# Performance work log

Hardware: AMD Instinct MI355X
Metric: run time of the kernel (lower is better)

Reference implementation:

```python
import jax, jax.numpy as jnp
import numpy as np

BN_EPS = 1e-5

def _conv1x1(x, w, b=None):
    # x: [B,C,H,W], w: [O,C] -> [B,O,H,W]
    y = jnp.einsum('bchw,oc->bohw', x, w)
    if b is not None:
        y = y + b[None, :, None, None]
    return y

def _bn_silu(y, gamma, beta):
    # BN inference with running_mean=0, running_var=1, then SiLU
    scale = gamma / jnp.sqrt(1.0 + BN_EPS)
    y = y * scale[None, :, None, None] + beta[None, :, None, None]
    return jax.nn.silu(y)

def setup_inputs() -> dict:
    key = jax.random.key(0)
    ks = jax.random.split(key, 20)
    B, D, S = 32, 512, 32
    C = D // 2
    d = {}
    d['x'] = jax.random.normal(ks[0], (B, D, S, S), jnp.float32)
    d['cv1_w'] = jax.random.normal(ks[1], (C, D), jnp.float32) * (1.0 / np.sqrt(D))
    d['cv1_gamma'] = jax.random.uniform(ks[2], (C,), jnp.float32, 0.5, 1.5)
    d['cv1_beta'] = jax.random.normal(ks[3], (C,), jnp.float32) * 0.1
    d['q_w'] = jax.random.normal(ks[4], (C, C), jnp.float32) * (1.0 / np.sqrt(C))
    d['q_b'] = jax.random.normal(ks[5], (C,), jnp.float32) * 0.02
    d['k_w'] = jax.random.normal(ks[6], (C, C), jnp.float32) * (1.0 / np.sqrt(C))
    d['k_b'] = jax.random.normal(ks[7], (C,), jnp.float32) * 0.02
    d['v_w'] = jax.random.normal(ks[8], (C, C), jnp.float32) * (1.0 / np.sqrt(C))
    d['v_b'] = jax.random.normal(ks[9], (C,), jnp.float32) * 0.02
    d['e_w'] = jax.random.normal(ks[10], (C, C), jnp.float32) * (1.0 / np.sqrt(C))
    d['e_b'] = jax.random.normal(ks[11], (C,), jnp.float32) * 0.02
    d['rel_h'] = jax.random.normal(ks[12], (1, C, S, 1), jnp.float32)
    d['rel_w'] = jax.random.normal(ks[13], (1, C, 1, S), jnp.float32)
    d['cv2_w'] = jax.random.normal(ks[14], (D, C), jnp.float32) * (1.0 / np.sqrt(C))
    d['cv2_gamma'] = jax.random.uniform(ks[15], (D,), jnp.float32, 0.5, 1.5)
    d['cv2_beta'] = jax.random.normal(ks[16], (D,), jnp.float32) * 0.1
    return d

def reference(x, cv1_w, cv1_gamma, cv1_beta, q_w, q_b, k_w, k_b, v_w, v_b,
              e_w, e_b, rel_h, rel_w, cv2_w, cv2_gamma, cv2_beta):
    # cv1: 1x1 conv (no bias) + BN + SiLU
    x1 = _bn_silu(_conv1x1(x, cv1_w), cv1_gamma, cv1_beta)  # [B,C,H,W]
    B, C, H, W = x1.shape
    N = H * W
    q = _conv1x1(x1, q_w, q_b).reshape(B, C, N)
    k = _conv1x1(x1, k_w, k_b).reshape(B, C, N)
    v = _conv1x1(x1, v_w, v_b).reshape(B, C, N)
    e = _conv1x1(x1, e_w, e_b).reshape(B, C, N)
    # content-content: q^T k -> [B,N,N]
    cc = jnp.einsum('bci,bcj->bij', q, k)
    # content-position: (rel_h + rel_w) flattened to [C,N], times extra proj
    pos = (rel_h + rel_w).reshape(C, N)  # broadcast add -> [1,C,H,W] -> [C,N]
    cp = jnp.einsum('ci,bcj->bij', pos, e)  # [B,N,N]
    attn = jax.nn.softmax(cc + cp, axis=-1)
    # out[b,c,i] = sum_j v[b,c,j] * attn[b,i,j]
    out = jnp.einsum('bcj,bij->bci', v, attn).reshape(B, C, H, W)
    y = _bn_silu(_conv1x1(out, cv2_w), cv2_gamma, cv2_beta)
    return x + y
```

## Files before the change

kernel.cpp:

```cpp
#include <hip/hip_runtime.h>
#include <hip/hip_bf16.h>

typedef unsigned short u16;
typedef __attribute__((ext_vector_type(8))) _Float16 half8;
typedef __attribute__((ext_vector_type(4))) float f32x4;

__device__ __forceinline__ u16 f2h(float f) {
  _Float16 h = (_Float16)f;
  union { _Float16 h; u16 u; } a; a.h = h;
  return a.u;
}

__device__ __forceinline__ float h2f(u16 u) {
  union { _Float16 h; u16 u; } a; a.u = u;
  return (float)a.h;
}

__device__ __forceinline__ float silu_f(float y) {
  return y / (1.0f + __expf(-y));
}

__device__ __forceinline__ void glds16(const u16* g, u16* l) {
  __builtin_amdgcn_global_load_lds(
      (__attribute__((address_space(1))) unsigned*)(g),
      (__attribute__((address_space(3))) unsigned*)(l), 16, 0, 0);
}

enum { EPI_BNSILU_N = 0, EPI_QKEV, EPI_RAW_F16, EPI_BNSILU_RES_M };

template<int EPI, bool DUAL, int TILES, int GX>
__global__ __launch_bounds__(256, 3)
void gemm_nt(const u16* __restrict__ A, long long a_bs, int lda,
             const u16* __restrict__ A2,
             const u16* __restrict__ B, long long b_bs, int ldb,
             void* __restrict__ C0, long long c_bs, int ldc,
             void* __restrict__ C1, void* __restrict__ C2,
             int K,
             const float* __restrict__ p0, const float* __restrict__ p1,
             const float* __restrict__ res, long long res_bs)
{
  __shared__ u16 smem[16384];

  const int id = blockIdx.x;
  const int bz = (id & 7) + 8 * (id / (8 * TILES));
  const int tt = (id >> 3) % TILES;
  const int bm = tt % GX;
  const int bn = tt / GX;
  const u16* Ab = A + (long long)bz * a_bs;
  const u16* Bb = B + (long long)bz * b_bs;
  const int m0 = bm * 128;
  const int n0 = bn * 128;
  const int t = threadIdx.x;
  const int lane = t & 63;
  const int w = t >> 6;
  const int wm = (w & 1) * 64;
  const int wn = (w >> 1) * 64;
  const int q = lane >> 4;
  const int lr = lane & 15;

  f32x4 acc[4][4];
#pragma unroll
  for (int i = 0; i < 4; ++i)
#pragma unroll
    for (int j = 0; j < 4; ++j)
      acc[i][j] = (f32x4){0.f, 0.f, 0.f, 0.f};

  const int lrow = lane >> 2;
  const int kch = (lane & 3) ^ ((lane >> 2) & 3) ^ ((lane >> 4) & 3);
  const int lk = kch * 8;
  const u16* aR0 = Ab + (long long)(m0 + 32 * w + lrow) * lda + lk;
  const u16* aR1 = aR0 + 16LL * lda;
  const u16* bR0 = Bb + (long long)(n0 + 32 * w + lrow) * ldb + lk;
  const u16* bR1 = bR0 + 16LL * ldb;
  const u16* a2R0 = nullptr; const u16* a2R1 = nullptr;
  if constexpr (DUAL) {
    a2R0 = A2 + (long long)(m0 + 32 * w + lrow) * 256 + lk;
    a2R1 = a2R0 + 16LL * 256;
  }
  u16* la0 = smem + w * 1024;        u16* la1 = la0 + 512;
  u16* lb0 = smem + 8192 + w * 1024; u16* lb1 = lb0 + 512;
  const int fpos = (q ^ (lr & 3) ^ ((lr >> 2) & 3)) * 8;

  for (int k0 = 0; k0 < K; k0 += 64) {
    __syncthreads();
    if (!DUAL || k0 < 256) {
      glds16(aR0 + k0, la0);        glds16(aR1 + k0, la1);
      glds16(aR0 + k0 + 32, la0 + 4096); glds16(aR1 + k0 + 32, la1 + 4096);
    } else {
      glds16(a2R0 + (k0 - 256), la0);        glds16(a2R1 + (k0 - 256), la1);
      glds16(a2R0 + (k0 - 224), la0 + 4096); glds16(a2R1 + (k0 - 224), la1 + 4096);
    }
    glds16(bR0 + k0, lb0);        glds16(bR1 + k0, lb1);
    glds16(bR0 + k0 + 32, lb0 + 4096); glds16(bR1 + k0 + 32, lb1 + 4096);
    __syncthreads();
#pragma unroll
    for (int h = 0; h < 2; ++h) {
      half8 af[4], bfr[4];
#pragma unroll
      for (int i = 0; i < 4; ++i)
        af[i] = *(const half8*)&smem[h * 4096 + (wm + i * 16 + lr) * 32 + fpos];
#pragma unroll
      for (int j = 0; j < 4; ++j)
        bfr[j] = *(const half8*)&smem[8192 + h * 4096 + (wn + j * 16 + lr) * 32 + fpos];
#pragma unroll
      for (int i = 0; i < 4; ++i)
#pragma unroll
        for (int j = 0; j < 4; ++j)
          acc[i][j] = __builtin_amdgcn_mfma_f32_16x16x32_f16(af[i], bfr[j], acc[i][j], 0, 0, 0);
    }
  }

  if constexpr (EPI == EPI_BNSILU_N) {
    u16* Cg = (u16*)C0 + (long long)bz * c_bs;
#pragma unroll
    for (int i = 0; i < 4; ++i)
#pragma unroll
      for (int j = 0; j < 4; ++j)
#pragma unroll
        for (int r = 0; r < 4; ++r) {
          const int m = m0 + wm + i * 16 + q * 4 + r;
          const int n = n0 + wn + j * 16 + lr;
          float v = acc[i][j][r];
          v = silu_f(v * (p0[n] * 0.99999500003749969f) + p1[n]);
          Cg[(long long)m * ldc + n] = f2h(v);
        }
  } else if constexpr (EPI == EPI_RAW_F16) {
    u16* Cg = (u16*)C0 + (long long)bz * c_bs;
#pragma unroll
    for (int i = 0; i < 4; ++i)
#pragma unroll
      for (int j = 0; j < 4; ++j)
#pragma unroll
        for (int r = 0; r < 4; ++r) {
          const int m = m0 + wm + i * 16 + q * 4 + r;
          const int n = n0 + wn + j * 16 + lr;
          Cg[(long long)m * ldc + n] = f2h(acc[i][j][r]);
        }
  } else if constexpr (EPI == EPI_BNSILU_RES_M) {
    float* Cg = (float*)C0 + (long long)bz * c_bs;
    const float* rg = res + (long long)bz * res_bs;
#pragma unroll
    for (int i = 0; i < 4; ++i)
#pragma unroll
      for (int j = 0; j < 4; ++j)
#pragma unroll
        for (int r = 0; r < 4; ++r) {
          const int m = m0 + wm + i * 16 + q * 4 + r;
          const int n = n0 + wn + j * 16 + lr;
          float v = acc[i][j][r];
          v = silu_f(v * (p0[m] * 0.99999500003749969f) + p1[m]);
          const long long idx = (long long)m * ldc + n;
          Cg[idx] = v + rg[idx];
        }
  } else {
    const int seg = n0 >> 8;
    const int nb = n0 & 255;
    if (seg < 3) {
      u16* dst; long long bs; int ld2;
      if (seg == 0) { dst = (u16*)C0; bs = 262144; ld2 = 256; }
      else { dst = (u16*)C1 + (seg == 2 ? 256 : 0); bs = 524288; ld2 = 512; }
      dst += (long long)bz * bs;
#pragma unroll
      for (int i = 0; i < 4; ++i)
#pragma unroll
        for (int j = 0; j < 4; ++j)
#pragma unroll
          for (int r = 0; r < 4; ++r) {
            const int m = m0 + wm + i * 16 + q * 4 + r;
            const int col = wn + j * 16 + lr;
            float v = acc[i][j][r] + p0[n0 + col];
            dst[(long long)m * ld2 + nb + col] = f2h(v);
          }
    } else {
      u16* dst = (u16*)C2 + (long long)bz * 262144;
#pragma unroll
      for (int s = 0; s < 4; ++s) {
        const int rbase = s * 32;
        __syncthreads();
        if (wm == (rbase & 64)) {
          const int ibase = (rbase & 32) >> 4;
#pragma unroll
          for (int ii = 0; ii < 2; ++ii) {
            const int i = ibase + ii;
#pragma unroll
            for (int j = 0; j < 4; ++j)
#pragma unroll
              for (int r = 0; r < 4; ++r) {
                const int row32 = i * 16 + q * 4 + r - (rbase & 32);
                const int col = wn + j * 16 + lr;
                float v = acc[i][j][r] + p0[768 + nb + col];
                smem[row32 * 132 + col] = f2h(v);
              }
          }
        }
        __syncthreads();
#pragma unroll
        for (int p = 0; p < 2; ++p) {
          const int lin = p * 256 + t;
          const int c = lin >> 2;
          const int mc = lin & 3;
          u16 tmp[8];
#pragma unroll
          for (int r8 = 0; r8 < 8; ++r8)
            tmp[r8] = smem[(mc * 8 + r8) * 132 + c];
          *(half8*)&dst[(long long)(nb + c) * 1024 + m0 + rbase + mc * 8] =
              *(const half8*)tmp;
        }
      }
    }
  }
}

__global__ __launch_bounds__(256)
void transpose_x(const float* __restrict__ x, u16* __restrict__ xT) {
  __shared__ float tile[64][33];
  const int b = blockIdx.z;
  const int n0 = blockIdx.x * 32;
  const int d0 = blockIdx.y * 64;
  const int tx = threadIdx.x;
  const int ty = threadIdx.y;
  const float* src = x + (long long)b * 524288;
#pragma unroll
  for (int i = 0; i < 8; ++i)
    tile[ty + 8 * i][tx] = src[(long long)(d0 + ty + 8 * i) * 1024 + n0 + tx];
  __syncthreads();
  u16* dst = xT + (long long)b * 524288;
#pragma unroll
  for (int i = 0; i < 4; ++i) {
    const int n = ty + 8 * i;
    unsigned lo = (unsigned)f2h(tile[2 * tx][n]);
    unsigned hi = (unsigned)f2h(tile[2 * tx + 1][n]);
    *(unsigned*)&dst[(long long)(n0 + n) * 512 + d0 + 2 * tx] = lo | (hi << 16);
  }
}

__global__ __launch_bounds__(256)
void convert_w(const float* __restrict__ w1, const float* __restrict__ wq,
               const float* __restrict__ wk, const float* __restrict__ wv,
               const float* __restrict__ we, const float* __restrict__ w2,
               const float* __restrict__ bq, const float* __restrict__ bk,
               const float* __restrict__ be, const float* __restrict__ bv,
               u16* __restrict__ dstw, float* __restrict__ bbuf) {
  int id = blockIdx.x * 256 + threadIdx.x;
  if (id < 524288) {
    float v;
    if (id < 131072) v = w1[id];
    else if (id < 393216) {
      int s = id - 131072, o = s >> 8, c = s & 255;
      if (o < 256) v = wq[o * 256 + c];
      else if (o < 512) v = wk[(o - 256) * 256 + c];
      else if (o < 768) v = we[(o - 512) * 256 + c];
      else v = wv[(o - 768) * 256 + c];
    } else v = w2[id - 393216];
    dstw[id] = f2h(v);
  } else {
    int i = id - 524288;
    float v;
    if (i < 256) v = bq[i];
    else if (i < 512) v = bk[i - 256];
    else if (i < 768) v = be[i - 512];
    else v = bv[i - 768];
    bbuf[i] = v;
  }
}

__global__ __launch_bounds__(256)
void pos_compute(const float* __restrict__ rh, const float* __restrict__ rw,
                 u16* __restrict__ posT) {
  const int n = blockIdx.x;
  const int c = threadIdx.x;
  posT[n * 256 + c] = f2h(rh[c * 32 + (n >> 5)] + rw[c * 32 + (n & 31)]);
}

__global__ __launch_bounds__(256)
void softmax_rows(u16* __restrict__ logits) {
  __shared__ float red[8];
  u16* p = logits + (long long)blockIdx.x * 1024;
  const int t = threadIdx.x;
  ushort4 raw = ((const ushort4*)p)[t];
  float v0 = h2f(raw.x), v1 = h2f(raw.y), v2 = h2f(raw.z), v3 = h2f(raw.w);
  float mx = fmaxf(fmaxf(v0, v1), fmaxf(v2, v3));
#pragma unroll
  for (int off = 32; off > 0; off >>= 1) mx = fmaxf(mx, __shfl_down(mx, off));
  const int lane = t & 63, w = t >> 6;
  if (lane == 0) red[w] = mx;
  __syncthreads();
  mx = fmaxf(fmaxf(red[0], red[1]), fmaxf(red[2], red[3]));
  float e0 = __expf(v0 - mx), e1 = __expf(v1 - mx),
        e2 = __expf(v2 - mx), e3 = __expf(v3 - mx);
  float s = e0 + e1 + e2 + e3;
#pragma unroll
  for (int off = 32; off > 0; off >>= 1) s += __shfl_down(s, off);
  if (lane == 0) red[4 + w] = s;
  __syncthreads();
  const float inv = 1.0f / (red[4] + red[5] + red[6] + red[7]);
  ushort4 o;
  o.x = f2h(e0 * inv); o.y = f2h(e1 * inv); o.z = f2h(e2 * inv); o.w = f2h(e3 * inv);
  ((ushort4*)p)[t] = o;
}

extern "C" void kernel_launch(void* const* d_in, const int* in_sizes, int n_in,
                              void* d_out, int out_size, void* d_ws, size_t ws_size,
                              hipStream_t stream) {
  const float* x  = (const float*)d_in[0];
  const float* w1 = (const float*)d_in[1];
  const float* g1 = (const float*)d_in[2];
  const float* b1 = (const float*)d_in[3];
  const float* wq = (const float*)d_in[4];
  const float* bq = (const float*)d_in[5];
  const float* wk = (const float*)d_in[6];
  const float* bk = (const float*)d_in[7];
  const float* wv = (const float*)d_in[8];
  const float* bv = (const float*)d_in[9];
  const float* we = (const float*)d_in[10];
  const float* be = (const float*)d_in[11];
  const float* rh = (const float*)d_in[12];
  const float* rw = (const float*)d_in[13];
  const float* w2 = (const float*)d_in[14];
  const float* g2 = (const float*)d_in[15];
  const float* b2 = (const float*)d_in[16];
  float* out = (float*)d_out;
  char* ws = (char*)d_ws;

  u16* xT     = (u16*)(ws + 0);
  u16* x1t    = (u16*)(ws + 33554432);
  u16* qbuf   = (u16*)(ws + 50331648);
  u16* kcat   = (u16*)(ws + 67108864);
  u16* vbuf   = (u16*)(ws + 100663296);
  u16* outt   = (u16*)(ws + 117440512);
  u16* posT   = (u16*)(ws + 134217728);
  u16* wbuf   = (u16*)(ws + 134742016);
  float* bbuf = (float*)(ws + 135790592);
  u16* logits = (u16*)(ws + 142606336);

  u16* w1b    = wbuf;
  u16* wqkve  = wbuf + 131072;
  u16* w2b    = wbuf + 393216;

  transpose_x<<<dim3(32, 8, 32), dim3(32, 8), 0, stream>>>(x, xT);
  convert_w<<<dim3(2052), 256, 0, stream>>>(w1, wq, wk, wv, we, w2,
                                            bq, bk, be, bv, wbuf, bbuf);
  pos_compute<<<dim3(1024), 256, 0, stream>>>(rh, rw, posT);

  gemm_nt<EPI_BNSILU_N, false, 16, 8><<<dim3(512), 256, 0, stream>>>(
      xT, 524288LL, 512, nullptr, w1b, 0LL, 512,
      x1t, 262144LL, 256, nullptr, nullptr, 512, g1, b1, nullptr, 0LL);

  gemm_nt<EPI_QKEV, false, 64, 8><<<dim3(2048), 256, 0, stream>>>(
      x1t, 262144LL, 256, nullptr, wqkve, 0LL, 256,
      qbuf, 262144LL, 256, kcat, vbuf, 256, bbuf, nullptr, nullptr, 0LL);

  gemm_nt<EPI_RAW_F16, true, 64, 8><<<dim3(2048), 256, 0, stream>>>(
      qbuf, 262144LL, 256, posT, kcat, 524288LL, 512,
      logits, 1048576LL, 1024, nullptr, nullptr, 512, nullptr, nullptr, nullptr, 0LL);

  softmax_rows<<<dim3(32768), 256, 0, stream>>>(logits);

  gemm_nt<EPI_RAW_F16, false, 16, 8><<<dim3(512), 256, 0, stream>>>(
      logits, 1048576LL, 1024, nullptr, vbuf, 262144LL, 1024,
      outt, 262144LL, 256, nullptr, nullptr, 1024, nullptr, nullptr, nullptr, 0LL);

  gemm_nt<EPI_BNSILU_RES_M, false, 32, 4><<<dim3(1024), 256, 0, stream>>>(
      w2b, 0LL, 256, nullptr, outt, 262144LL, 256,
      out, 524288LL, 1024, nullptr, nullptr, 256, g2, b2, x, 524288LL);
}
```

Baseline: 330.7 us.

## Fuse softmax exponentiation and normalization into the attention-times-V GEMM

The softmax pass no longer rewrites the logits. It now only computes a per-row max and sum and stores them as a float2 stats buffer. The attn·V GEMM exponentiates the A fragments on the fly using the row max and scales the output by the inverse row sum in its epilogue. This removes a full read-modify-write of the fp16 logits tensor, at the cost of extra exp work inside the GEMM's inner loop. Each logits element is exponentiated once per N-tile, so this is repeated across tiles.

Result: slower. 352.2 us (+6.5%).

```diff
diff --git a/kernel.cpp b/kernel.cpp
--- a/kernel.cpp
+++ b/kernel.cpp
@@ -26,7 +26,7 @@
       (__attribute__((address_space(3))) unsigned*)(l), 16, 0, 0);
 }
 
-enum { EPI_BNSILU_N = 0, EPI_QKEV, EPI_RAW_F16, EPI_BNSILU_RES_M };
+enum { EPI_BNSILU_N = 0, EPI_QKEV, EPI_RAW_F16, EPI_BNSILU_RES_M, EPI_ATTNV };
 
 template<int EPI, bool DUAL, int TILES, int GX>
 __global__ __launch_bounds__(256, 3)
@@ -81,6 +81,13 @@
   u16* lb0 = smem + 8192 + w * 1024; u16* lb1 = lb0 + 512;
   const int fpos = (q ^ (lr & 3) ^ ((lr >> 2) & 3)) * 8;
 
+  float mrow[4] = {0.f, 0.f, 0.f, 0.f};
+  if constexpr (EPI == EPI_ATTNV) {
+    const float2* st = (const float2*)p0 + (long long)bz * 1024;
+#pragma unroll
+    for (int i = 0; i < 4; ++i) mrow[i] = st[m0 + wm + i * 16 + lr].x;
+  }
+
   for (int k0 = 0; k0 < K; k0 += 64) {
     __syncthreads();
     if (!DUAL || k0 < 256) {
@@ -102,6 +109,15 @@
 #pragma unroll
       for (int j = 0; j < 4; ++j)
         bfr[j] = *(const half8*)&smem[8192 + h * 4096 + (wn + j * 16 + lr) * 32 + fpos];
+      if constexpr (EPI == EPI_ATTNV) {
+#pragma unroll
+        for (int i = 0; i < 4; ++i)
+#pragma unroll
+          for (int e = 0; e < 8; ++e) {
+            float f = (float)af[i][e];
+            af[i][e] = (_Float16)__expf(f - mrow[i]);
+          }
+      }
 #pragma unroll
       for (int i = 0; i < 4; ++i)
 #pragma unroll
@@ -136,6 +152,21 @@
           const int n = n0 + wn + j * 16 + lr;
           Cg[(long long)m * ldc + n] = f2h(acc[i][j][r]);
         }
+  } else if constexpr (EPI == EPI_ATTNV) {
+    u16* Cg = (u16*)C0 + (long long)bz * c_bs;
+    const float2* st = (const float2*)p0 + (long long)bz * 1024;
+#pragma unroll
+    for (int i = 0; i < 4; ++i)
+#pragma unroll
+      for (int r = 0; r < 4; ++r) {
+        const int m = m0 + wm + i * 16 + q * 4 + r;
+        const float linv = 1.0f / st[m].y;
+#pragma unroll
+        for (int j = 0; j < 4; ++j) {
+          const int n = n0 + wn + j * 16 + lr;
+          Cg[(long long)m * ldc + n] = f2h(acc[i][j][r] * linv);
+        }
+      }
   } else if constexpr (EPI == EPI_BNSILU_RES_M) {
     float* Cg = (float*)C0 + (long long)bz * c_bs;
     const float* rg = res + (long long)bz * res_bs;
@@ -273,9 +304,9 @@
 }
 
 __global__ __launch_bounds__(256)
-void softmax_rows(u16* __restrict__ logits) {
+void softmax_stats(const u16* __restrict__ logits, float2* __restrict__ stats) {
   __shared__ float red[8];
-  u16* p = logits + (long long)blockIdx.x * 1024;
+  const u16* p = logits + (long long)blockIdx.x * 1024;
   const int t = threadIdx.x;
   ushort4 raw = ((const ushort4*)p)[t];
   float v0 = h2f(raw.x), v1 = h2f(raw.y), v2 = h2f(raw.z), v3 = h2f(raw.w);
@@ -286,17 +317,13 @@
   if (lane == 0) red[w] = mx;
   __syncthreads();
   mx = fmaxf(fmaxf(red[0], red[1]), fmaxf(red[2], red[3]));
-  float e0 = __expf(v0 - mx), e1 = __expf(v1 - mx),
-        e2 = __expf(v2 - mx), e3 = __expf(v3 - mx);
-  float s = e0 + e1 + e2 + e3;
+  float s = __expf(v0 - mx) + __expf(v1 - mx) + __expf(v2 - mx) + __expf(v3 - mx);
 #pragma unroll
   for (int off = 32; off > 0; off >>= 1) s += __shfl_down(s, off);
   if (lane == 0) red[4 + w] = s;
   __syncthreads();
-  const float inv = 1.0f / (red[4] + red[5] + red[6] + red[7]);
-  ushort4 o;
-  o.x = f2h(e0 * inv); o.y = f2h(e1 * inv); o.z = f2h(e2 * inv); o.w = f2h(e3 * inv);
-  ((ushort4*)p)[t] = o;
+  if (t == 0)
+    stats[blockIdx.x] = make_float2(mx, red[4] + red[5] + red[6] + red[7]);
 }
 
 extern "C" void kernel_launch(void* const* d_in, const int* in_sizes, int n_in,
@@ -331,6 +358,7 @@
   u16* posT   = (u16*)(ws + 134217728);
   u16* wbuf   = (u16*)(ws + 134742016);
   float* bbuf = (float*)(ws + 135790592);
+  float* stats= (float*)(ws + 136314880);
   u16* logits = (u16*)(ws + 142606336);
 
   u16* w1b    = wbuf;
@@ -354,11 +382,11 @@
       qbuf, 262144LL, 256, posT, kcat, 524288LL, 512,
       logits, 1048576LL, 1024, nullptr, nullptr, 512, nullptr, nullptr, nullptr, 0LL);
 
-  softmax_rows<<<dim3(32768), 256, 0, stream>>>(logits);
-
-  gemm_nt<EPI_RAW_F16, false, 16, 8><<<dim3(512), 256, 0, stream>>>(
+  softmax_stats<<<dim3(32768), 256, 0, stream>>>(logits, (float2*)stats);
+
+  gemm_nt<EPI_ATTNV, false, 16, 8><<<dim3(512), 256, 0, stream>>>(
       logits, 1048576LL, 1024, nullptr, vbuf, 262144LL, 1024,
-      outt, 262144LL, 256, nullptr, nullptr, 1024, nullptr, nullptr, nullptr, 0LL);
+      outt, 262144LL, 256, nullptr, nullptr, 1024, stats, nullptr, nullptr, 0LL);
 
   gemm_nt<EPI_BNSILU_RES_M, false, 32, 4><<<dim3(1024), 256, 0, stream>>>(
       w2b, 0LL, 256, nullptr, outt, 262144LL, 256,
```
